# Optimization experiments

Hardware: AMD Instinct MI355X
Metric: run time of the kernel (lower is better)

The kernel has to match this reference:

```python
import jax, jax.numpy as jnp
import numpy as np

ALPHA = 0.6
K = 4


def gsdnef_conv(x, edge_index, W, b, alpha, K):
    """SpGSDNEFConv: linear transform then K-step graph-signal-denoising diffusion
    h_{k+1} = (x + alpha * A_hat h_k) / (1 + alpha), A_hat = D^-1/2 (A+I) D^-1/2."""
    n = x.shape[0]
    x = x @ W + b  # [N, C_out]
    loop = jnp.arange(n, dtype=edge_index.dtype)
    src = jnp.concatenate([edge_index[0], loop])
    dst = jnp.concatenate([edge_index[1], loop])
    ones = jnp.ones(src.shape, dtype=x.dtype)
    deg = jax.ops.segment_sum(ones, dst, num_segments=n)
    dinv = jax.lax.rsqrt(jnp.maximum(deg, 1e-12))
    norm = dinv[src] * dinv[dst]  # [E+N]
    inv = 1.0 / (1.0 + alpha)
    h = x
    for _ in range(K):
        agg = jax.ops.segment_sum(h[src] * norm[:, None], dst, num_segments=n)
        h = (x + alpha * agg) * inv
    return h


def setup_inputs() -> dict:
    key = jax.random.key(0)
    ks = jax.random.split(key, 16)
    N, E, C_in, H, C_out = 50000, 800000, 256, 128, 64
    x = jax.random.normal(ks[0], (N, C_in), dtype=jnp.float32)
    edge_index = jax.random.randint(ks[1], (2, E), 0, N, dtype=jnp.int64)

    def lin(k, fan_in, fan_out):
        k1, k2 = jax.random.split(k)
        bound = 1.0 / np.sqrt(fan_in)
        W = jax.random.uniform(k1, (fan_in, fan_out), jnp.float32, -bound, bound)
        b = jax.random.uniform(k2, (fan_out,), jnp.float32, -bound, bound)
        return W, b

    Wc1, bc1 = lin(ks[2], C_in, H)
    Wl1, bl1 = lin(ks[3], C_in, H)
    Wc2, bc2 = lin(ks[4], H, H)
    Wl2, bl2 = lin(ks[5], H, H)
    Wc3, bc3 = lin(ks[6], H, C_out)
    Wl3, bl3 = lin(ks[7], H, C_out)
    return dict(x=x, edge_index=edge_index,
                Wc1=Wc1, bc1=bc1, Wl1=Wl1, bl1=bl1,
                Wc2=Wc2, bc2=bc2, Wl2=Wl2, bl2=bl2,
                Wc3=Wc3, bc3=bc3, Wl3=Wl3, bl3=bl3)


def reference(x, edge_index, Wc1, bc1, Wl1, bl1, Wc2, bc2, Wl2, bl2, Wc3, bc3, Wl3, bl3):
    h = jax.nn.elu(gsdnef_conv(x, edge_index, Wc1, bc1, ALPHA, K) + (x @ Wl1 + bl1))
    h = jax.nn.elu(gsdnef_conv(h, edge_index, Wc2, bc2, ALPHA, K) + (h @ Wl2 + bl2))
    h = gsdnef_conv(h, edge_index, Wc3, bc3, ALPHA, K) + (h @ Wl3 + bl3)
    return h
```

## Files before the change

kernel.cpp:

```cpp
#include <hip/hip_runtime.h>
#include <hip/hip_fp16.h>
#include <math.h>

#define ALPHA_C 0.6f

typedef _Float16 f16;
typedef f16 f16x8 __attribute__((ext_vector_type(8)));
typedef float f32x4 __attribute__((ext_vector_type(4)));

__global__ void f32_to_f16_kernel(const float* __restrict__ in, f16* __restrict__ out, int n8) {
    int i = blockIdx.x * blockDim.x + threadIdx.x;
    if (i >= n8) return;
    float4 a = ((const float4*)in)[2 * i];
    float4 b = ((const float4*)in)[2 * i + 1];
    f16x8 o;
    o[0] = (f16)a.x; o[1] = (f16)a.y; o[2] = (f16)a.z; o[3] = (f16)a.w;
    o[4] = (f16)b.x; o[5] = (f16)b.y; o[6] = (f16)b.z; o[7] = (f16)b.w;
    ((f16x8*)out)[i] = o;
}

__global__ void detect_idx_kernel(const void* __restrict__ ei, int* __restrict__ flag,
                                  int E, int N) {
    int i = blockIdx.x * blockDim.x + threadIdx.x;
    if (i >= E) return;
    long long v = ((const long long*)ei)[i];
    if (v < 0 || v >= (long long)N) *flag = 1;
}

__global__ void convert_count_kernel(const void* __restrict__ ei, const int* __restrict__ flag,
                                     int* __restrict__ out, int* __restrict__ cnt,
                                     int E, int n2e) {
    int i = blockIdx.x * blockDim.x + threadIdx.x;
    if (i >= n2e) return;
    int v;
    if (*flag == 0)
        v = (int)((const long long*)ei)[i];
    else
        v = ((const int*)ei)[i];
    out[i] = v;
    if (i >= E) atomicAdd(&cnt[v], 1);
}

__global__ void block_reduce_kernel(const int* __restrict__ cnt, int* __restrict__ bsum,
                                    float* __restrict__ dinv, int n) {
    __shared__ int s[256];
    int tid = threadIdx.x;
    int i = blockIdx.x * 256 + tid;
    int v = (i < n) ? cnt[i] : 0;
    if (i < n) dinv[i] = rsqrtf((float)v + 1.0f);
    s[tid] = v;
    __syncthreads();
    for (int o = 128; o > 0; o >>= 1) {
        if (tid < o) s[tid] += s[tid + o];
        __syncthreads();
    }
    if (tid == 0) bsum[blockIdx.x] = s[0];
}

__global__ void scan_top_kernel(int* __restrict__ bsum, int nb) {
    __shared__ int s[1024];
    int tid = threadIdx.x;
    int v = (tid < nb) ? bsum[tid] : 0;
    s[tid] = v;
    __syncthreads();
    for (int o = 1; o < 1024; o <<= 1) {
        int t = (tid >= o) ? s[tid - o] : 0;
        __syncthreads();
        s[tid] += t;
        __syncthreads();
    }
    if (tid < nb) bsum[tid] = s[tid] - v;
}

__global__ void scan_fill_kernel(const int* __restrict__ cnt, const int* __restrict__ bsum,
                                 int* __restrict__ row_off, int n) {
    __shared__ int s[256];
    int tid = threadIdx.x;
    int i = blockIdx.x * 256 + tid;
    int v = (i < n) ? cnt[i] : 0;
    s[tid] = v;
    __syncthreads();
    for (int o = 1; o < 256; o <<= 1) {
        int t = (tid >= o) ? s[tid - o] : 0;
        __syncthreads();
        s[tid] += t;
        __syncthreads();
    }
    int base = bsum[blockIdx.x];
    if (i < n) row_off[i] = base + s[tid] - v;
    if (i == n - 1) row_off[n] = base + s[tid];
}

__global__ void fill_kernel(const int* __restrict__ src, const int* __restrict__ dst,
                            const float* __restrict__ dinv, const int* __restrict__ row_off,
                            int* __restrict__ cursor, unsigned int* __restrict__ csre, int E) {
    int e = blockIdx.x * blockDim.x + threadIdx.x;
    if (e >= E) return;
    int d = dst[e], s = src[e];
    int pos = atomicAdd(&cursor[d], 1);
    int idx = row_off[d] + pos;
    float w = dinv[s] * dinv[d];
    csre[idx] = (unsigned int)s |
                ((unsigned int)__half_as_ushort(__float2half(w)) << 16);
}

__global__ void prep_all_w_kernel(
    const float* __restrict__ Wc1, const float* __restrict__ Wl1,
    const float* __restrict__ Wc2, const float* __restrict__ Wl2,
    const float* __restrict__ Wc3, const float* __restrict__ Wl3,
    f16* __restrict__ w1c, f16* __restrict__ w1l,
    f16* __restrict__ w2c, f16* __restrict__ w2l,
    f16* __restrict__ w3c, f16* __restrict__ w3l) {
    int i = blockIdx.x * blockDim.x + threadIdx.x;
    const float* W; f16* O; int K, Nn, base;
    if      (i <  32768) { W = Wc1; O = w1c; K = 256; Nn = 128; base = i; }
    else if (i <  65536) { W = Wl1; O = w1l; K = 256; Nn = 128; base = i - 32768; }
    else if (i <  81920) { W = Wc2; O = w2c; K = 128; Nn = 128; base = i - 65536; }
    else if (i <  98304) { W = Wl2; O = w2l; K = 128; Nn = 128; base = i - 81920; }
    else if (i < 106496) { W = Wc3; O = w3c; K = 128; Nn = 64;  base = i - 98304; }
    else if (i < 114688) { W = Wl3; O = w3l; K = 128; Nn = 64;  base = i - 106496; }
    else return;
    int k = base / Nn, n = base - k * Nn;
    O[(size_t)n * K + k] = (f16)W[base];
}

template <int K, int NH, int AMODE, int SPLIT>
__global__ __launch_bounds__(256) void gemm2_kernel(
    const void* __restrict__ A0v, const void* __restrict__ A1v,
    const f16* __restrict__ WtA, const f16* __restrict__ WtB,
    const float* __restrict__ biasA, const float* __restrict__ biasB,
    f16* __restrict__ CA, f16* __restrict__ CB, int M) {
    constexpr int NT = 2 * NH / 16;
    constexpr int NTS = NT / SPLIT;
    constexpr int KS = K / 32;
    __shared__ f16 Wlds[NTS * 1024];

    int tid = threadIdx.x;
    int wv = tid >> 6, lane = tid & 63;
    int lr = lane & 15, lhi = lane >> 4;
    int m0 = blockIdx.x * 64;
    int tg0 = blockIdx.y * NTS;

    f32x4 acc[NTS];
#pragma unroll
    for (int t = 0; t < NTS; ++t) acc[t] = (f32x4){0.f, 0.f, 0.f, 0.f};

    int arow = m0 + wv * 16 + lr;
    int arow_c = arow < M ? arow : M - 1;
    size_t aoff = (size_t)arow_c * K + lhi * 8;

    f16x8 a[KS];
#pragma unroll
    for (int j = 0; j < KS; ++j) {
        size_t idx = aoff + j * 32;
        if constexpr (AMODE == 0) {
            a[j] = *(const f16x8*)((const f16*)A0v + idx);
        } else {
            f16x8 u0 = *(const f16x8*)((const f16*)A0v + idx);
            f16x8 u1 = *(const f16x8*)((const f16*)A1v + idx);
            f16x8 v;
#pragma unroll
            for (int jj = 0; jj < 8; ++jj) {
                float tt = (float)u0[jj] + (float)u1[jj];
                v[jj] = (f16)(tt > 0.f ? tt : expm1f(tt));
            }
            a[j] = v;
        }
    }

#pragma unroll
    for (int k0 = 0; k0 < K; k0 += 64) {
        for (int c = tid; c < NTS * 128; c += 256) {
            int tl = c >> 7;
            int rem = c & 127;
            int ks = rem >> 6, kh = (rem >> 4) & 3, r = rem & 15;
            int tg = tg0 + tl;
            int nloc = (tg < NT / 2) ? tg : tg - NT / 2;
            const f16* srcp = ((tg < NT / 2) ? WtA : WtB)
                              + (size_t)(nloc * 16 + r) * K + k0 + ks * 32 + kh * 8;
            *(f16x8*)&Wlds[(size_t)c * 8] = *(const f16x8*)srcp;
        }
        __syncthreads();

#pragma unroll
        for (int s2 = 0; s2 < 2; ++s2) {
#pragma unroll
            for (int t = 0; t < NTS; ++t) {
                f16x8 b = *(const f16x8*)&Wlds[(size_t)(t * 128 + s2 * 64 + lane) * 8];
                acc[t] = __builtin_amdgcn_mfma_f32_16x16x32_f16(a[k0 / 32 + s2], b, acc[t], 0, 0, 0);
            }
        }
        __syncthreads();
    }

    int rbase = m0 + wv * 16 + lhi * 4;
#pragma unroll
    for (int t = 0; t < NTS; ++t) {
        int tg = tg0 + t;
        bool isA = (tg < NT / 2);
        int colg = (isA ? tg : tg - NT / 2) * 16 + lr;
        f16* outp = isA ? CA : CB;
        float bv = (isA ? biasA : biasB)[colg];
#pragma unroll
        for (int r = 0; r < 4; ++r) {
            int row = rbase + r;
            if (row < M) outp[(size_t)row * NH + colg] = (f16)(acc[t][r] + bv);
        }
    }
}

template <int C, bool FINAL>
__global__ __launch_bounds__(256) void diffuse16_kernel(
    const __half* __restrict__ h, const __half* __restrict__ xc,
    const float* __restrict__ dinv, const int* __restrict__ row_off,
    const unsigned int* __restrict__ csre, __half* __restrict__ hout,
    const f16* __restrict__ lin, float* __restrict__ fout, int N) {
    const float inv = 1.0f / (1.0f + ALPHA_C);
    int gid = blockIdx.x * blockDim.x + threadIdx.x;
    int node = gid >> 6;
    if (node >= N) return;
    int lane = threadIdx.x & 63;
    float di = dinv[node];
    float di2 = di * di;
    int e0 = row_off[node], e1 = row_off[node + 1];

    if constexpr (C == 128) {
        int l = lane & 15, grp = lane >> 4;
        float acc[8];
#pragma unroll
        for (int i = 0; i < 8; ++i) acc[i] = 0.f;
        size_t coff = (size_t)l * 8;

        if (grp == 0) {
            float4 rv = *(const float4*)(h + ((size_t)node << 7) + coff);
            const __half2* p = (const __half2*)&rv;
#pragma unroll
            for (int k = 0; k < 4; ++k) {
                float2 f = __half22float2(p[k]);
                acc[2 * k] += di2 * f.x;
                acc[2 * k + 1] += di2 * f.y;
            }
        }
        int e = e0 + grp;
        for (; e + 12 < e1; e += 16) {
            unsigned int ev0 = csre[e], ev1 = csre[e + 4], ev2 = csre[e + 8], ev3 = csre[e + 12];
            float4 r0 = *(const float4*)(h + ((size_t)(ev0 & 0xFFFF) << 7) + coff);
            float4 r1 = *(const float4*)(h + ((size_t)(ev1 & 0xFFFF) << 7) + coff);
            float4 r2 = *(const float4*)(h + ((size_t)(ev2 & 0xFFFF) << 7) + coff);
            float4 r3 = *(const float4*)(h + ((size_t)(ev3 & 0xFFFF) << 7) + coff);
            float w0 = __half2float(__ushort_as_half((unsigned short)(ev0 >> 16)));
            float w1 = __half2float(__ushort_as_half((unsigned short)(ev1 >> 16)));
            float w2 = __half2float(__ushort_as_half((unsigned short)(ev2 >> 16)));
            float w3 = __half2float(__ushort_as_half((unsigned short)(ev3 >> 16)));
            const __half2* p0 = (const __half2*)&r0;
            const __half2* p1 = (const __half2*)&r1;
            const __half2* p2 = (const __half2*)&r2;
            const __half2* p3 = (const __half2*)&r3;
#pragma unroll
            for (int k = 0; k < 4; ++k) {
                float2 f0 = __half22float2(p0[k]);
                float2 f1 = __half22float2(p1[k]);
                float2 f2 = __half22float2(p2[k]);
                float2 f3 = __half22float2(p3[k]);
                acc[2 * k]     += w0 * f0.x + w1 * f1.x + w2 * f2.x + w3 * f3.x;
                acc[2 * k + 1] += w0 * f0.y + w1 * f1.y + w2 * f2.y + w3 * f3.y;
            }
        }
        for (; e < e1; e += 4) {
            unsigned int ev0 = csre[e];
            float4 r0 = *(const float4*)(h + ((size_t)(ev0 & 0xFFFF) << 7) + coff);
            float w0 = __half2float(__ushort_as_half((unsigned short)(ev0 >> 16)));
            const __half2* p0 = (const __half2*)&r0;
#pragma unroll
            for (int k = 0; k < 4; ++k) {
                float2 f0 = __half22float2(p0[k]);
                acc[2 * k]     += w0 * f0.x;
                acc[2 * k + 1] += w0 * f0.y;
            }
        }
#pragma unroll
        for (int i = 0; i < 8; ++i) {
            acc[i] += __shfl_xor(acc[i], 16);
            acc[i] += __shfl_xor(acc[i], 32);
        }
        if (grp == 0) {
            float4 xv = *(const float4*)(xc + ((size_t)node << 7) + coff);
            const __half2* xp = (const __half2*)&xv;
            __half ov[8];
#pragma unroll
            for (int k = 0; k < 4; ++k) {
                float2 xf = __half22float2(xp[k]);
                ov[2 * k]     = __float2half((xf.x + ALPHA_C * acc[2 * k]) * inv);
                ov[2 * k + 1] = __float2half((xf.y + ALPHA_C * acc[2 * k + 1]) * inv);
            }
            *(float4*)(hout + ((size_t)node << 7) + coff) = *(float4*)ov;
        }
    } else {
        int l = lane & 7, grp = lane >> 3;
        float acc[8];
#pragma unroll
        for (int i = 0; i < 8; ++i) acc[i] = 0.f;
        size_t coff = (size_t)l * 8;

        if (grp == 0) {
            float4 rv = *(const float4*)(h + ((size_t)node << 6) + coff);
            const __half2* p = (const __half2*)&rv;
#pragma unroll
            for (int k = 0; k < 4; ++k) {
                float2 f = __half22float2(p[k]);
                acc[2 * k] += di2 * f.x;
                acc[2 * k + 1] += di2 * f.y;
            }
        }
        int e = e0 + grp;
        for (; e + 8 < e1; e += 16) {
            unsigned int ev0 = csre[e], ev1 = csre[e + 8];
            float4 r0 = *(const float4*)(h + ((size_t)(ev0 & 0xFFFF) << 6) + coff);
            float4 r1 = *(const float4*)(h + ((size_t)(ev1 & 0xFFFF) << 6) + coff);
            float w0 = __half2float(__ushort_as_half((unsigned short)(ev0 >> 16)));
            float w1 = __half2float(__ushort_as_half((unsigned short)(ev1 >> 16)));
            const __half2* p0 = (const __half2*)&r0;
            const __half2* p1 = (const __half2*)&r1;
#pragma unroll
            for (int k = 0; k < 4; ++k) {
                float2 f0 = __half22float2(p0[k]);
                float2 f1 = __half22float2(p1[k]);
                acc[2 * k]     += w0 * f0.x + w1 * f1.x;
                acc[2 * k + 1] += w0 * f0.y + w1 * f1.y;
            }
        }
        if (e < e1) {
            unsigned int ev0 = csre[e];
            float4 r0 = *(const float4*)(h + ((size_t)(ev0 & 0xFFFF) << 6) + coff);
            float w0 = __half2float(__ushort_as_half((unsigned short)(ev0 >> 16)));
            const __half2* p0 = (const __half2*)&r0;
#pragma unroll
            for (int k = 0; k < 4; ++k) {
                float2 f0 = __half22float2(p0[k]);
                acc[2 * k]     += w0 * f0.x;
                acc[2 * k + 1] += w0 * f0.y;
            }
        }
#pragma unroll
        for (int i = 0; i < 8; ++i) {
            acc[i] += __shfl_xor(acc[i], 8);
            acc[i] += __shfl_xor(acc[i], 16);
            acc[i] += __shfl_xor(acc[i], 32);
        }
        if (grp == 0) {
            float4 xv = *(const float4*)(xc + ((size_t)node << 6) + coff);
            const __half2* xp = (const __half2*)&xv;
            float r[8];
#pragma unroll
            for (int k = 0; k < 4; ++k) {
                float2 xf = __half22float2(xp[k]);
                r[2 * k]     = (xf.x + ALPHA_C * acc[2 * k]) * inv;
                r[2 * k + 1] = (xf.y + ALPHA_C * acc[2 * k + 1]) * inv;
            }
            if constexpr (FINAL) {
                f16x8 lv = *(const f16x8*)(lin + ((size_t)node << 6) + coff);
                float4 o0, o1;
                o0.x = r[0] + (float)lv[0]; o0.y = r[1] + (float)lv[1];
                o0.z = r[2] + (float)lv[2]; o0.w = r[3] + (float)lv[3];
                o1.x = r[4] + (float)lv[4]; o1.y = r[5] + (float)lv[5];
                o1.z = r[6] + (float)lv[6]; o1.w = r[7] + (float)lv[7];
                float* op = fout + ((size_t)node << 6) + coff;
                *(float4*)op = o0;
                *(float4*)(op + 4) = o1;
            } else {
                __half ov[8];
#pragma unroll
                for (int k = 0; k < 8; ++k) ov[k] = __float2half(r[k]);
                *(float4*)(hout + ((size_t)node << 6) + coff) = *(float4*)ov;
            }
        }
    }
}

extern "C" void kernel_launch(void* const* d_in, const int* in_sizes, int n_in,
                              void* d_out, int out_size, void* d_ws, size_t ws_size,
                              hipStream_t stream) {
    const float* x   = (const float*)d_in[0];
    const void*  ei  = d_in[1];
    const float* Wc1 = (const float*)d_in[2];  const float* bc1 = (const float*)d_in[3];
    const float* Wl1 = (const float*)d_in[4];  const float* bl1 = (const float*)d_in[5];
    const float* Wc2 = (const float*)d_in[6];  const float* bc2 = (const float*)d_in[7];
    const float* Wl2 = (const float*)d_in[8];  const float* bl2 = (const float*)d_in[9];
    const float* Wc3 = (const float*)d_in[10]; const float* bc3 = (const float*)d_in[11];
    const float* Wl3 = (const float*)d_in[12]; const float* bl3 = (const float*)d_in[13];
    float* out = (float*)d_out;

    const int N = in_sizes[0] / 256;
    const int E = in_sizes[1] / 2;

    size_t off = 0;
    auto alloc = [&](size_t bytes) {
        void* p = (char*)d_ws + off;
        off += (bytes + 255) & ~(size_t)255;
        return p;
    };
    f16* x16 = (f16*)alloc((size_t)N * 256 * 2);
    f16* B0 = (f16*)alloc((size_t)N * 128 * 2);
    f16* B1 = (f16*)alloc((size_t)N * 128 * 2);
    f16* B2 = (f16*)alloc((size_t)N * 128 * 2);
    f16* B3 = (f16*)alloc((size_t)N * 128 * 2);
    f16* B4 = (f16*)alloc((size_t)N * 128 * 2);
    f16* wt1c = (f16*)alloc((size_t)256 * 128 * 2);
    f16* wt1l = (f16*)alloc((size_t)256 * 128 * 2);
    f16* wt2c = (f16*)alloc((size_t)128 * 128 * 2);
    f16* wt2l = (f16*)alloc((size_t)128 * 128 * 2);
    f16* wt3c = (f16*)alloc((size_t)128 * 64 * 2);
    f16* wt3l = (f16*)alloc((size_t)128 * 64 * 2);
    float* dinv   = (float*)alloc((size_t)N * 4);
    int*   zreg   = (int*)  alloc((size_t)(2 * N + 64) * 4);
    int*   flag   = zreg;
    int*   cnt    = zreg + 64;
    int*   cursor = zreg + 64 + N;
    int*   rowoff = (int*)  alloc((size_t)(N + 1) * 4);
    int*   bsum   = (int*)  alloc(1024 * 4);
    unsigned int* csre = (unsigned int*)alloc((size_t)E * 4);
    int*   idx32  = (int*)  alloc((size_t)2 * E * 4);
    int* src32 = idx32;
    int* dst32 = idx32 + E;

    const int TB = 256;
    int ge  = (E + TB - 1) / TB;
    int g2e = (2 * E + TB - 1) / TB;
    int nb  = (N + 255) / 256;

    hipMemsetAsync(zreg, 0, (size_t)(2 * N + 64) * 4, stream);

    int gx8 = (N * 256 / 8 + TB - 1) / TB;
    f32_to_f16_kernel<<<gx8, TB, 0, stream>>>(x, x16, N * 256 / 8);

    detect_idx_kernel<<<ge, TB, 0, stream>>>(ei, flag, E, N);
    convert_count_kernel<<<g2e, TB, 0, stream>>>(ei, flag, idx32, cnt, E, 2 * E);

    block_reduce_kernel<<<nb, 256, 0, stream>>>(cnt, bsum, dinv, N);
    scan_top_kernel<<<1, 1024, 0, stream>>>(bsum, nb);
    scan_fill_kernel<<<nb, 256, 0, stream>>>(cnt, bsum, rowoff, N);
    fill_kernel<<<ge, TB, 0, stream>>>(src32, dst32, dinv, rowoff, cursor, csre, E);

    prep_all_w_kernel<<<(114688 + TB - 1) / TB, TB, 0, stream>>>(
        Wc1, Wl1, Wc2, Wl2, Wc3, Wl3, wt1c, wt1l, wt2c, wt2l, wt3c, wt3l);

    dim3 gm((N + 63) / 64, 2);
    int gd = (N * 64 + TB - 1) / TB;

    gemm2_kernel<256, 128, 0, 2><<<gm, TB, 0, stream>>>(x16, nullptr, wt1c, wt1l, bc1, bl1, B0, B1, N);
    diffuse16_kernel<128, false><<<gd, TB, 0, stream>>>((__half*)B0, (__half*)B0, dinv, rowoff, csre, (__half*)B2, nullptr, nullptr, N);
    diffuse16_kernel<128, false><<<gd, TB, 0, stream>>>((__half*)B2, (__half*)B0, dinv, rowoff, csre, (__half*)B3, nullptr, nullptr, N);
    diffuse16_kernel<128, false><<<gd, TB, 0, stream>>>((__half*)B3, (__half*)B0, dinv, rowoff, csre, (__half*)B2, nullptr, nullptr, N);
    diffuse16_kernel<128, false><<<gd, TB, 0, stream>>>((__half*)B2, (__half*)B0, dinv, rowoff, csre, (__half*)B3, nullptr, nullptr, N);

    gemm2_kernel<128, 128, 2, 2><<<gm, TB, 0, stream>>>(B3, B1, wt2c, wt2l, bc2, bl2, B0, B4, N);
    diffuse16_kernel<128, false><<<gd, TB, 0, stream>>>((__half*)B0, (__half*)B0, dinv, rowoff, csre, (__half*)B1, nullptr, nullptr, N);
    diffuse16_kernel<128, false><<<gd, TB, 0, stream>>>((__half*)B1, (__half*)B0, dinv, rowoff, csre, (__half*)B2, nullptr, nullptr, N);
    diffuse16_kernel<128, false><<<gd, TB, 0, stream>>>((__half*)B2, (__half*)B0, dinv, rowoff, csre, (__half*)B1, nullptr, nullptr, N);
    diffuse16_kernel<128, false><<<gd, TB, 0, stream>>>((__half*)B1, (__half*)B0, dinv, rowoff, csre, (__half*)B2, nullptr, nullptr, N);

    gemm2_kernel<128, 64, 2, 2><<<gm, TB, 0, stream>>>(B2, B4, wt3c, wt3l, bc3, bl3, B0, B1, N);
    diffuse16_kernel<64, false><<<gd, TB, 0, stream>>>((__half*)B0, (__half*)B0, dinv, rowoff, csre, (__half*)B2, nullptr, nullptr, N);
    diffuse16_kernel<64, false><<<gd, TB, 0, stream>>>((__half*)B2, (__half*)B0, dinv, rowoff, csre, (__half*)B3, nullptr, nullptr, N);
    diffuse16_kernel<64, false><<<gd, TB, 0, stream>>>((__half*)B3, (__half*)B0, dinv, rowoff, csre, (__half*)B2, nullptr, nullptr, N);
    diffuse16_kernel<64, true ><<<gd, TB, 0, stream>>>((__half*)B2, (__half*)B0, dinv, rowoff, csre, nullptr, B1, out, N);
}
```

Before: 559.1 us.

## Build CSR via two-pass bucketed scatter instead of per-edge global atomics

Replaces the per-edge global atomic CSR fill with a two-stage bucket sort. Edges are first binned into 64-node buckets using shared-memory histograms and one global atomic per bucket per block. Each bucket is then finalized in shared memory with local atomics and computed weights. The aim is to cut random global atomics and scattered writes. It adds an extra edge buffer pass, and it assumes node ids fit in 16 bits and that there are at most 1024 buckets.

```diff
diff --git a/kernel.cpp b/kernel.cpp
--- a/kernel.cpp
+++ b/kernel.cpp
@@ -73,7 +73,7 @@
 }
 
 __global__ void scan_fill_kernel(const int* __restrict__ cnt, const int* __restrict__ bsum,
-                                 int* __restrict__ row_off, int n) {
+                                 int* __restrict__ row_off, int* __restrict__ gcur, int n) {
     __shared__ int s[256];
     int tid = threadIdx.x;
     int i = blockIdx.x * 256 + tid;
@@ -87,21 +87,92 @@
         __syncthreads();
     }
     int base = bsum[blockIdx.x];
-    if (i < n) row_off[i] = base + s[tid] - v;
+    if (i < n) {
+        int ro = base + s[tid] - v;
+        row_off[i] = ro;
+        if ((i & 63) == 0) gcur[i >> 6] = ro;
+    }
     if (i == n - 1) row_off[n] = base + s[tid];
 }
 
-__global__ void fill_kernel(const int* __restrict__ src, const int* __restrict__ dst,
-                            const float* __restrict__ dinv, const int* __restrict__ row_off,
-                            int* __restrict__ cursor, unsigned int* __restrict__ csre, int E) {
-    int e = blockIdx.x * blockDim.x + threadIdx.x;
-    if (e >= E) return;
-    int d = dst[e], s = src[e];
-    int pos = atomicAdd(&cursor[d], 1);
-    int idx = row_off[d] + pos;
-    float w = dinv[s] * dinv[d];
-    csre[idx] = (unsigned int)s |
-                ((unsigned int)__half_as_ushort(__float2half(w)) << 16);
+__global__ __launch_bounds__(256) void bucket_scatter_kernel(
+    const int* __restrict__ src, const int* __restrict__ dst,
+    int* __restrict__ gcur, unsigned int* __restrict__ ebuf, int E, int NB) {
+    __shared__ int hist[1024];
+    __shared__ int loff[1024];
+    __shared__ int lbase[1024];
+    __shared__ int lcur[1024];
+    __shared__ unsigned int lbuf[8192];
+    int tid = threadIdx.x;
+    int e0 = blockIdx.x * 8192;
+    int ecnt = E - e0; if (ecnt > 8192) ecnt = 8192;
+
+    for (int i = tid; i < 1024; i += 256) { hist[i] = 0; lcur[i] = 0; }
+    __syncthreads();
+    for (int i = tid; i < ecnt; i += 256)
+        atomicAdd(&hist[(unsigned)dst[e0 + i] >> 6], 1);
+    __syncthreads();
+    for (int i = tid; i < 1024; i += 256) loff[i] = hist[i];
+    __syncthreads();
+    for (int o = 1; o < 1024; o <<= 1) {
+        int v[4];
+#pragma unroll
+        for (int r = 0; r < 4; ++r) { int i = tid + r * 256; v[r] = (i >= o) ? loff[i - o] : 0; }
+        __syncthreads();
+#pragma unroll
+        for (int r = 0; r < 4; ++r) { int i = tid + r * 256; loff[i] += v[r]; }
+        __syncthreads();
+    }
+    for (int b = tid; b < NB; b += 256) {
+        int h = hist[b];
+        lbase[b] = h ? atomicAdd(&gcur[b], h) : 0;
+    }
+    __syncthreads();
+    for (int i = tid; i < ecnt; i += 256) {
+        int d = dst[e0 + i], s = src[e0 + i];
+        int b = (unsigned)d >> 6;
+        int p = atomicAdd(&lcur[b], 1);
+        lbuf[loff[b] - hist[b] + p] = (unsigned)s | ((unsigned)d << 16);
+    }
+    __syncthreads();
+    int wave = tid >> 6, lane = tid & 63;
+    for (int b = wave; b < NB; b += 4) {
+        int h = hist[b];
+        int lo = loff[b] - h;
+        int gb = lbase[b];
+        for (int j = lane; j < h; j += 64) ebuf[gb + j] = lbuf[lo + j];
+    }
+}
+
+__global__ __launch_bounds__(256) void csr_finalize_kernel(
+    const unsigned int* __restrict__ ebuf, const int* __restrict__ row_off,
+    const float* __restrict__ dinv, unsigned int* __restrict__ csre, int N) {
+    __shared__ int lcur[64];
+    __shared__ unsigned int lbuf[2048];
+    int b = blockIdx.x;
+    int n0 = b * 64;
+    int n1 = n0 + 64; if (n1 > N) n1 = N;
+    int base = row_off[n0];
+    int cnt = row_off[n1] - base;
+    int tid = threadIdx.x;
+    if (tid < 64) lcur[tid] = 0;
+    __syncthreads();
+    bool fits = (cnt <= 2048);
+    for (int i = tid; i < cnt; i += 256) {
+        unsigned int pr = ebuf[base + i];
+        int s = pr & 0xFFFF;
+        int d = pr >> 16;
+        float w = dinv[s] * dinv[d];
+        unsigned int entry = (unsigned)s |
+                             ((unsigned)__half_as_ushort(__float2half(w)) << 16);
+        int rel = row_off[d] - base;
+        int p = atomicAdd(&lcur[d - n0], 1);
+        if (fits) lbuf[rel + p] = entry;
+        else      csre[base + rel + p] = entry;
+    }
+    __syncthreads();
+    if (fits)
+        for (int i = tid; i < cnt; i += 256) csre[base + i] = lbuf[i];
 }
 
 __global__ void prep_all_w_kernel(
@@ -392,6 +463,7 @@
 
     const int N = in_sizes[0] / 256;
     const int E = in_sizes[1] / 2;
+    const int NB = (N + 63) >> 6;
 
     size_t off = 0;
     auto alloc = [&](size_t bytes) {
@@ -412,13 +484,14 @@
     f16* wt3c = (f16*)alloc((size_t)128 * 64 * 2);
     f16* wt3l = (f16*)alloc((size_t)128 * 64 * 2);
     float* dinv   = (float*)alloc((size_t)N * 4);
-    int*   zreg   = (int*)  alloc((size_t)(2 * N + 64) * 4);
+    int*   zreg   = (int*)  alloc((size_t)(N + 64) * 4);
     int*   flag   = zreg;
     int*   cnt    = zreg + 64;
-    int*   cursor = zreg + 64 + N;
     int*   rowoff = (int*)  alloc((size_t)(N + 1) * 4);
     int*   bsum   = (int*)  alloc(1024 * 4);
+    int*   gcur   = (int*)  alloc(1024 * 4);
     unsigned int* csre = (unsigned int*)alloc((size_t)E * 4);
+    unsigned int* ebuf = (unsigned int*)alloc((size_t)E * 4);
     int*   idx32  = (int*)  alloc((size_t)2 * E * 4);
     int* src32 = idx32;
     int* dst32 = idx32 + E;
@@ -428,7 +501,7 @@
     int g2e = (2 * E + TB - 1) / TB;
     int nb  = (N + 255) / 256;
 
-    hipMemsetAsync(zreg, 0, (size_t)(2 * N + 64) * 4, stream);
+    hipMemsetAsync(zreg, 0, (size_t)(N + 64) * 4, stream);
 
     int gx8 = (N * 256 / 8 + TB - 1) / TB;
     f32_to_f16_kernel<<<gx8, TB, 0, stream>>>(x, x16, N * 256 / 8);
@@ -438,8 +511,10 @@
 
     block_reduce_kernel<<<nb, 256, 0, stream>>>(cnt, bsum, dinv, N);
     scan_top_kernel<<<1, 1024, 0, stream>>>(bsum, nb);
-    scan_fill_kernel<<<nb, 256, 0, stream>>>(cnt, bsum, rowoff, N);
-    fill_kernel<<<ge, TB, 0, stream>>>(src32, dst32, dinv, rowoff, cursor, csre, E);
+    scan_fill_kernel<<<nb, 256, 0, stream>>>(cnt, bsum, rowoff, gcur, N);
+    int gbk = (E + 8191) / 8192;
+    bucket_scatter_kernel<<<gbk, 256, 0, stream>>>(src32, dst32, gcur, ebuf, E, NB);
+    csr_finalize_kernel<<<NB, 256, 0, stream>>>(ebuf, rowoff, dinv, csre, N);
 
     prep_all_w_kernel<<<(114688 + TB - 1) / TB, TB, 0, stream>>>(
         Wc1, Wl1, Wc2, Wl2, Wc3, Wl3, wt1c, wt1l, wt2c, wt2l, wt3c, wt3l);
```

Measured after the change: 582.3 us. 4.1% more time.
